# Optimization experiments

Hardware: AMD Instinct MI355X
Metric: run time of the kernel (lower is better)

Reference implementation:

```python
import jax, jax.numpy as jnp
import numpy as np

BAND_WIDTH = 0.5
EPS = 1e-5


def setup_inputs() -> dict:
    key = jax.random.key(0)
    k1, k2 = jax.random.split(key)
    shape = (8, 128, 16, 16, 16)  # (N, C, H, W, D)
    x = jax.random.normal(k1, shape, dtype=jnp.float32)
    y = jax.random.normal(k2, shape, dtype=jnp.float32)
    return {"x": x, "y": y}


def reference(x, y):
    N, C = x.shape[0], x.shape[1]
    L = x.shape[2] * x.shape[3] * x.shape[4]  # H*W*D
    xr = x.reshape(N, C, L)
    yr = y.reshape(N, C, L)
    # center by target mean over (batch, spatial)
    y_mu = yr.mean(axis=(0, 2), keepdims=True)  # (1, C, 1)
    xc = xr - y_mu
    yc = yr - y_mu
    # L2 normalize along channel dim (torch F.normalize: eps=1e-12 clamp on norm)
    xn = xc / jnp.maximum(jnp.linalg.norm(xc, axis=1, keepdims=True), 1e-12)
    yn = yc / jnp.maximum(jnp.linalg.norm(yc, axis=1, keepdims=True), 1e-12)
    # cosine similarity matrix (N, L, L): rows index x positions, cols y positions
    cos = jnp.einsum('ncl,ncm->nlm', xn, yn)
    dist = 1.0 - cos
    dist_min = jnp.min(dist, axis=2, keepdims=True)  # (N, L, 1)
    dist_tilde = dist / (dist_min + EPS)
    cx = jax.nn.softmax((1.0 - dist_tilde) / BAND_WIDTH, axis=2)
    cx = jnp.mean(jnp.max(cx, axis=1), axis=1)  # (N,)
    loss = jnp.mean(-jnp.log(cx + EPS))
    return loss
```

## Files before the change

kernel.cpp:

```cpp
#include <hip/hip_runtime.h>
#include <math.h>


#define NB 8
#define CC 128
#define LL 4096
#define CL (CC * LL)
#define EPSV 1e-5f
#define L2E 1.44269504f
#define TWO_L2E 2.88539008f

typedef __bf16 bf16x8 __attribute__((ext_vector_type(8)));
typedef float f32x4 __attribute__((ext_vector_type(4)));

__device__ __forceinline__ unsigned short f2bf(float f) {
    unsigned u = __float_as_uint(f);
    u += 0x7FFFu + ((u >> 16) & 1u);
    return (unsigned short)(u >> 16);
}

__global__ void k_mu1(const float* __restrict__ y, float* __restrict__ muP, float* __restrict__ out) {
    const int b = blockIdx.x;
    const int t = threadIdx.x;
    if (b == 0 && t == 0) out[0] = 0.f;
    const float* p = y + (size_t)b * LL;
    float4 v0 = *(const float4*)(p + t * 4);
    float4 v1 = *(const float4*)(p + 1024 + t * 4);
    float4 v2 = *(const float4*)(p + 2048 + t * 4);
    float4 v3 = *(const float4*)(p + 3072 + t * 4);
    float s = (v0.x + v0.y + v0.z + v0.w) + (v1.x + v1.y + v1.z + v1.w)
            + (v2.x + v2.y + v2.z + v2.w) + (v3.x + v3.y + v3.z + v3.w);
    for (int o = 1; o < 64; o <<= 1) s += __shfl_xor(s, o, 64);
    __shared__ float red[4];
    if ((t & 63) == 0) red[t >> 6] = s;
    __syncthreads();
    if (t == 0) muP[b] = (red[0] + red[1]) + (red[2] + red[3]);
}

__global__ __launch_bounds__(256, 2) void k_prep(const float* __restrict__ x, const float* __restrict__ y,
                                                 const float* __restrict__ muP,
                                                 unsigned short* __restrict__ xt, unsigned short* __restrict__ yt) {
    __shared__ float tf[CC][132];
    __shared__ float ssq[2][CC];
    __shared__ float invn[CC];
    __shared__ float mu_s[CC];
    const int b = blockIdx.x;
    const float* src = (b & 256) ? y : x;
    unsigned short* dst = (b & 256) ? yt : xt;
    const int sub = b & 255;
    const int n = sub >> 5, l0 = (sub & 31) << 7;
    const int t = threadIdx.x;
    if (t < CC) {
        float s = 0.f;
#pragma unroll
        for (int nn = 0; nn < NB; ++nn) s += muP[nn * CC + t];
        mu_s[t] = s * (1.0f / (float)(NB * LL));
    }
    const float* g = src + (size_t)n * CL + l0;
#pragma unroll
    for (int it = 0; it < 16; ++it) {
        int id = (it << 8) + t;
        int c = id >> 5, l4 = (id & 31) << 2;
        *(float4*)&tf[c][l4] = *(const float4*)(g + (size_t)c * LL + l4);
    }
    __syncthreads();
    {
        const int l = t & 127, half = t >> 7;
        float ss = 0.f;
#pragma unroll
        for (int cc = 0; cc < 64; ++cc) {
            int c = (half << 6) + cc;
            float v = tf[c][l] - mu_s[c];
            tf[c][l] = v;
            ss += v * v;
        }
        ssq[half][l] = ss;
    }
    __syncthreads();
    if (t < CC) invn[t] = 1.0f / fmaxf(sqrtf(ssq[0][t] + ssq[1][t]), 1e-12f);
    __syncthreads();
    unsigned short* o = dst + ((size_t)n * LL + l0) * CC;
#pragma unroll
    for (int it = 0; it < 8; ++it) {
        int id = (it << 8) + t;
        int lr = id >> 4, c8 = (id & 15) << 3;
        float w = invn[lr];
        unsigned short h[8] __attribute__((aligned(16)));
#pragma unroll
        for (int j = 0; j < 8; ++j) h[j] = f2bf(tf[c8 + j][lr] * w);
        *(uint4*)&o[(size_t)lr * CC + c8] = *(uint4*)h;
    }
}

__device__ __forceinline__ void stage_dma(const unsigned short* __restrict__ g,
                                          unsigned short* lds, int t) {
    const int w = t >> 6, ln = t & 63;
#pragma unroll
    for (int c = 0; c < 8; ++c) {
        int rbase = w * 32 + c * 4;
        int row = rbase + (ln >> 4);
        int gg = (ln & 15) ^ (row & 15);
        const unsigned short* gp = g + ((size_t)row << 7) + (gg << 3);
        __builtin_amdgcn_global_load_lds(
            (const __attribute__((address_space(1))) void*)gp,
            (__attribute__((address_space(3))) void*)(lds + (rbase << 7)),
            16, 0, 0);
    }
}

__device__ __forceinline__ bf16x8 ldsfrag(const unsigned short* lds, int r, int kq) {
    return *(const bf16x8*)&lds[(r << 7) + ((kq ^ (r & 15)) << 3)];
}

__device__ __forceinline__ void gather_frags(const unsigned short* __restrict__ g,
                                             bf16x8 (&areg)[4][4], int row0, int lane) {
    const int mr = lane & 15, q = lane >> 4;
    const unsigned short* ab = g + ((size_t)(row0 + mr) << 7) + q * 8;
#pragma unroll
    for (int k0i = 0; k0i < 4; ++k0i)
#pragma unroll
        for (int i = 0; i < 4; ++i)
            areg[k0i][i] = *(const bf16x8*)(ab + ((size_t)(i * 16) << 7) + k0i * 32);
}

__device__ __forceinline__ void mfma_stream(const bf16x8 (&areg)[4][4], const unsigned short* Bs,
                                            f32x4 (&acc)[4][4], int col0, int lane) {
    const int mr = lane & 15, q = lane >> 4;
#pragma unroll
    for (int k0i = 0; k0i < 4; ++k0i) {
        bf16x8 b[4];
#pragma unroll
        for (int j = 0; j < 4; ++j)
            b[j] = ldsfrag(Bs, col0 + j * 16 + mr, 4 * k0i + q);
#pragma unroll
        for (int i = 0; i < 4; ++i)
#pragma unroll
            for (int j = 0; j < 4; ++j)
                acc[i][j] = __builtin_amdgcn_mfma_f32_16x16x32_bf16(areg[k0i][i], b[j], acc[i][j], 0, 0, 0);
    }
}


#define DECODE_B(b, n_, lt_, ms_)                          \
    const int xcd_ = (b) & 7, slot_ = (b) >> 3;            \
    const int grp_ = xcd_ * 4 + (slot_ >> 5);              \
    const int n_ = grp_ >> 2, ms_ = grp_ & 3, lt_ = slot_ & 31;

__global__ __launch_bounds__(256, 2) void k_rowmax(const unsigned short* __restrict__ xt,
                                                   const unsigned short* __restrict__ yt,
                                                   float* __restrict__ rmP) {
    __shared__ unsigned short Bs[CC * CC];
    DECODE_B(blockIdx.x, n, lt, ms)
    const int t = threadIdx.x, lane = t & 63, w = t >> 6;
    const int row0 = (w & 1) << 6, col0 = (w >> 1) << 6;
    const int q = lane >> 4;
    bf16x8 areg[4][4];
    gather_frags(xt + ((size_t)(n * LL + lt * 128) << 7), areg, row0, lane);
    float rmax[16];
#pragma unroll
    for (int v = 0; v < 16; ++v) rmax[v] = -1e30f;
    for (int mt = ms * 8; mt < ms * 8 + 8; ++mt) {
        __syncthreads();
        stage_dma(yt + ((size_t)(n * LL + mt * 128) << 7), Bs, t);
        __syncthreads();
        f32x4 acc[4][4];
#pragma unroll
        for (int i = 0; i < 4; ++i)
#pragma unroll
            for (int j = 0; j < 4; ++j) acc[i][j] = 0.f;
        mfma_stream(areg, Bs, acc, col0, lane);
#pragma unroll
        for (int i = 0; i < 4; ++i)
#pragma unroll
            for (int r = 0; r < 4; ++r) {
                float m = acc[i][0][r];
#pragma unroll
                for (int j = 1; j < 4; ++j) m = fmaxf(m, acc[i][j][r]);
                rmax[i * 4 + r] = fmaxf(rmax[i * 4 + r], m);
            }
    }
#pragma unroll
    for (int v = 0; v < 16; ++v) {
        rmax[v] = fmaxf(rmax[v], __shfl_xor(rmax[v], 1, 64));
        rmax[v] = fmaxf(rmax[v], __shfl_xor(rmax[v], 2, 64));
        rmax[v] = fmaxf(rmax[v], __shfl_xor(rmax[v], 4, 64));
        rmax[v] = fmaxf(rmax[v], __shfl_xor(rmax[v], 8, 64));
    }
    if ((lane & 15) == 0) {
        const int part = ms * 2 + (w >> 1);
#pragma unroll
        for (int v = 0; v < 16; ++v) {
            int row = lt * 128 + row0 + (v >> 2) * 16 + q * 4 + (v & 3);
            rmP[((size_t)part << 15) + n * LL + row] = rmax[v];
        }
    }
}

__global__ __launch_bounds__(256, 2) void k_z(const unsigned short* __restrict__ xt,
                                              const unsigned short* __restrict__ yt,
                                              const float* __restrict__ rmP,
                                              float* __restrict__ Zp) {
    __shared__ unsigned short Bs[CC * CC];
    __shared__ float b2s[CC];
    DECODE_B(blockIdx.x, n, lt, ms)
    const int t = threadIdx.x, lane = t & 63, w = t >> 6;
    const int row0 = (w & 1) << 6, col0 = (w >> 1) << 6;
    const int q = lane >> 4;
    if (t < CC) {
        size_t gi = (size_t)n * LL + lt * 128 + t;
        float rm = -1e30f;
#pragma unroll
        for (int p = 0; p < 8; ++p) rm = fmaxf(rm, rmP[gi + ((size_t)p << 15)]);
        b2s[t] = (2.0f / (1.0f - rm + EPSV)) * L2E;
    }
    bf16x8 areg[4][4];
    gather_frags(xt + ((size_t)(n * LL + lt * 128) << 7), areg, row0, lane);
    __syncthreads();
    float b2[16], zs[16];
#pragma unroll
    for (int v = 0; v < 16; ++v) {
        b2[v] = b2s[row0 + (v >> 2) * 16 + q * 4 + (v & 3)];
        zs[v] = 0.f;
    }
    for (int mt = ms * 8; mt < ms * 8 + 8; ++mt) {
        __syncthreads();
        stage_dma(yt + ((size_t)(n * LL + mt * 128) << 7), Bs, t);
        __syncthreads();
        f32x4 acc[4][4];
#pragma unroll
        for (int i = 0; i < 4; ++i)
#pragma unroll
            for (int j = 0; j < 4; ++j) acc[i][j] = 0.f;
        mfma_stream(areg, Bs, acc, col0, lane);
#pragma unroll
        for (int i = 0; i < 4; ++i)
#pragma unroll
            for (int r = 0; r < 4; ++r) {
                int v = i * 4 + r;
                float e2v = TWO_L2E - b2[v];
                float s = 0.f;
#pragma unroll
                for (int j = 0; j < 4; ++j)
                    s += __builtin_amdgcn_exp2f(fmaf(b2[v], acc[i][j][r], e2v));
                zs[v] += s;
            }
    }
#pragma unroll
    for (int v = 0; v < 16; ++v) {
        zs[v] += __shfl_xor(zs[v], 1, 64);
        zs[v] += __shfl_xor(zs[v], 2, 64);
        zs[v] += __shfl_xor(zs[v], 4, 64);
        zs[v] += __shfl_xor(zs[v], 8, 64);
    }
    if ((lane & 15) == 0) {
        const int part = ms * 2 + (w >> 1);
#pragma unroll
        for (int v = 0; v < 16; ++v) {
            int row = lt * 128 + row0 + (v >> 2) * 16 + q * 4 + (v & 3);
            Zp[((size_t)part << 15) + n * LL + row] = zs[v];
        }
    }
}

__global__ __launch_bounds__(256, 2) void k_colmax(const unsigned short* __restrict__ xt,
                                                   const unsigned short* __restrict__ yt,
                                                   const float* __restrict__ rmP, const float* __restrict__ Zp,
                                                   float* __restrict__ cmP) {
    __shared__ unsigned short Bs[CC * CC];
    __shared__ float b2s[1024], g2s[1024];
    DECODE_B(blockIdx.x, n, ct, ls)
    const int t = threadIdx.x, lane = t & 63, w = t >> 6;
    const int row0 = (w & 1) << 6, col0 = (w >> 1) << 6;
    const int mr = lane & 15, q = lane >> 4;
    for (int i = t; i < 1024; i += 256) {
        size_t gi = (size_t)n * LL + ls * 1024 + i;
        float rm = -1e30f;
#pragma unroll
        for (int p = 0; p < 8; ++p) rm = fmaxf(rm, rmP[gi + ((size_t)p << 15)]);
        float b2 = (2.0f / (1.0f - rm + EPSV)) * L2E;
        float Z = 0.f;
#pragma unroll
        for (int p = 0; p < 8; ++p) Z += Zp[gi + ((size_t)p << 15)];
        b2s[i] = b2;
        g2s[i] = (TWO_L2E - b2) - __builtin_amdgcn_logf(Z);
    }
    bf16x8 areg[4][4];
    gather_frags(yt + ((size_t)(n * LL + ct * 128) << 7), areg, row0, lane);
    float cmax[16];
#pragma unroll
    for (int v = 0; v < 16; ++v) cmax[v] = -1e30f;
    for (int lt = ls * 8; lt < ls * 8 + 8; ++lt) {
        __syncthreads();
        stage_dma(xt + ((size_t)(n * LL + lt * 128) << 7), Bs, t);
        __syncthreads();
        f32x4 acc[4][4];
#pragma unroll
        for (int i = 0; i < 4; ++i)
#pragma unroll
            for (int j = 0; j < 4; ++j) acc[i][j] = 0.f;
        mfma_stream(areg, Bs, acc, col0, lane);
        float b2v[4], g2v[4];
        const int lbase = (lt - ls * 8) * 128 + col0 + mr;
#pragma unroll
        for (int j = 0; j < 4; ++j) {
            b2v[j] = b2s[lbase + j * 16];
            g2v[j] = g2s[lbase + j * 16];
        }
#pragma unroll
        for (int i = 0; i < 4; ++i)
#pragma unroll
            for (int r = 0; r < 4; ++r) {
                int v = i * 4 + r;
                float m = cmax[v];
#pragma unroll
                for (int j = 0; j < 4; ++j)
                    m = fmaxf(m, fmaf(b2v[j], acc[i][j][r], g2v[j]));
                cmax[v] = m;
            }
    }
#pragma unroll
    for (int v = 0; v < 16; ++v) {
        cmax[v] = fmaxf(cmax[v], __shfl_xor(cmax[v], 1, 64));
        cmax[v] = fmaxf(cmax[v], __shfl_xor(cmax[v], 2, 64));
        cmax[v] = fmaxf(cmax[v], __shfl_xor(cmax[v], 4, 64));
        cmax[v] = fmaxf(cmax[v], __shfl_xor(cmax[v], 8, 64));
    }
    if (mr == 0) {
        const int part = ls * 2 + (w >> 1);
#pragma unroll
        for (int v = 0; v < 16; ++v) {
            int yc = ct * 128 + row0 + (v >> 2) * 16 + q * 4 + (v & 3);
            cmP[((size_t)part << 15) + n * LL + yc] = cmax[v];
        }
    }
}

__global__ void k_loss(const float* __restrict__ cmP, float* __restrict__ out) {
    __shared__ float red[256];
    const int n = blockIdx.x, t = threadIdx.x;
    float s = 0.f;
    for (int m = t; m < LL; m += 256) {
        size_t idx = (size_t)n * LL + m;
        float e = -1e30f;
#pragma unroll
        for (int p = 0; p < 8; ++p) e = fmaxf(e, cmP[idx + ((size_t)p << 15)]);
        s += __builtin_amdgcn_exp2f(e);
    }
    red[t] = s;
    __syncthreads();
    for (int o = 128; o > 0; o >>= 1) {
        if (t < o) red[t] += red[t + o];
        __syncthreads();
    }
    if (t == 0)
        atomicAdd(out, -logf(red[0] * (1.0f / (float)LL) + EPSV) * (1.0f / (float)NB));
}

extern "C" void kernel_launch(void* const* d_in, const int* in_sizes, int n_in,
                              void* d_out, int out_size, void* d_ws, size_t ws_size,
                              hipStream_t stream) {
    const float* x = (const float*)d_in[0];
    const float* y = (const float*)d_in[1];
    float* out = (float*)d_out;
    char* ws = (char*)d_ws;

    unsigned short* xt = (unsigned short*)ws;
    unsigned short* yt = (unsigned short*)(ws + 8388608);
    char* p = ws + 16777216;
    float* muP = (float*)p;            p += 4096;
    float* rmP = (float*)p;            p += 8 * 131072;
    float* Zp  = (float*)p;            p += 8 * 131072;
    float* cmP = rmP;

    k_mu1<<<1024, 256, 0, stream>>>(y, muP, out);
    k_prep<<<512, 256, 0, stream>>>(x, y, muP, xt, yt);
    k_rowmax<<<1024, 256, 0, stream>>>(xt, yt, rmP);
    k_z<<<1024, 256, 0, stream>>>(xt, yt, rmP, Zp);
    k_colmax<<<1024, 256, 0, stream>>>(xt, yt, rmP, Zp, cmP);
    k_loss<<<8, 256, 0, stream>>>(cmP, out);
}
```

Measured before the change: 208.8 us.

## Load B fragments directly from global memory, halve grid with longer tile loops

Removes the LDS staging (global_load_lds DMA plus two barriers per tile) and has each wave read its B operand fragments straight from global memory. The three GEMM kernels now run 512 blocks, each covering 16 column tiles instead of 8, so the partial-result buffers shrink from 8 to 4 parts and cmP gets its own buffer. The goal is to drop barrier and LDS overhead, but B data is no longer shared through LDS, so L2 traffic rises and global load latency is exposed without double buffering.

```diff
diff --git a/kernel.cpp b/kernel.cpp
--- a/kernel.cpp
+++ b/kernel.cpp
@@ -92,26 +92,6 @@
     }
 }
 
-__device__ __forceinline__ void stage_dma(const unsigned short* __restrict__ g,
-                                          unsigned short* lds, int t) {
-    const int w = t >> 6, ln = t & 63;
-#pragma unroll
-    for (int c = 0; c < 8; ++c) {
-        int rbase = w * 32 + c * 4;
-        int row = rbase + (ln >> 4);
-        int gg = (ln & 15) ^ (row & 15);
-        const unsigned short* gp = g + ((size_t)row << 7) + (gg << 3);
-        __builtin_amdgcn_global_load_lds(
-            (const __attribute__((address_space(1))) void*)gp,
-            (__attribute__((address_space(3))) void*)(lds + (rbase << 7)),
-            16, 0, 0);
-    }
-}
-
-__device__ __forceinline__ bf16x8 ldsfrag(const unsigned short* lds, int r, int kq) {
-    return *(const bf16x8*)&lds[(r << 7) + ((kq ^ (r & 15)) << 3)];
-}
-
 __device__ __forceinline__ void gather_frags(const unsigned short* __restrict__ g,
                                              bf16x8 (&areg)[4][4], int row0, int lane) {
     const int mr = lane & 15, q = lane >> 4;
@@ -123,52 +103,50 @@
             areg[k0i][i] = *(const bf16x8*)(ab + ((size_t)(i * 16) << 7) + k0i * 32);
 }
 
-__device__ __forceinline__ void mfma_stream(const bf16x8 (&areg)[4][4], const unsigned short* Bs,
-                                            f32x4 (&acc)[4][4], int col0, int lane) {
-    const int mr = lane & 15, q = lane >> 4;
+__device__ __forceinline__ void mfma_direct(const bf16x8 (&areg)[4][4],
+                                            const unsigned short* __restrict__ bp,
+                                            f32x4 (&acc)[4][4]) {
 #pragma unroll
     for (int k0i = 0; k0i < 4; ++k0i) {
-        bf16x8 b[4];
+        bf16x8 bb[4];
 #pragma unroll
         for (int j = 0; j < 4; ++j)
-            b[j] = ldsfrag(Bs, col0 + j * 16 + mr, 4 * k0i + q);
+            bb[j] = *(const bf16x8*)(bp + ((size_t)(j * 16) << 7) + k0i * 32);
 #pragma unroll
         for (int i = 0; i < 4; ++i)
 #pragma unroll
             for (int j = 0; j < 4; ++j)
-                acc[i][j] = __builtin_amdgcn_mfma_f32_16x16x32_bf16(areg[k0i][i], b[j], acc[i][j], 0, 0, 0);
-    }
-}
-
-
-#define DECODE_B(b, n_, lt_, ms_)                          \
+                acc[i][j] = __builtin_amdgcn_mfma_f32_16x16x32_bf16(areg[k0i][i], bb[j], acc[i][j], 0, 0, 0);
+    }
+}
+
+
+#define DECODE_512(b, n_, lt_, ms_)                        \
     const int xcd_ = (b) & 7, slot_ = (b) >> 3;            \
-    const int grp_ = xcd_ * 4 + (slot_ >> 5);              \
-    const int n_ = grp_ >> 2, ms_ = grp_ & 3, lt_ = slot_ & 31;
+    const int grp_ = xcd_ * 2 + (slot_ >> 5);              \
+    const int n_ = grp_ >> 1, ms_ = grp_ & 1, lt_ = slot_ & 31;
 
 __global__ __launch_bounds__(256, 2) void k_rowmax(const unsigned short* __restrict__ xt,
                                                    const unsigned short* __restrict__ yt,
                                                    float* __restrict__ rmP) {
-    __shared__ unsigned short Bs[CC * CC];
-    DECODE_B(blockIdx.x, n, lt, ms)
+    DECODE_512(blockIdx.x, n, lt, ms)
     const int t = threadIdx.x, lane = t & 63, w = t >> 6;
     const int row0 = (w & 1) << 6, col0 = (w >> 1) << 6;
-    const int q = lane >> 4;
+    const int mr = lane & 15, q = lane >> 4;
     bf16x8 areg[4][4];
     gather_frags(xt + ((size_t)(n * LL + lt * 128) << 7), areg, row0, lane);
     float rmax[16];
 #pragma unroll
     for (int v = 0; v < 16; ++v) rmax[v] = -1e30f;
-    for (int mt = ms * 8; mt < ms * 8 + 8; ++mt) {
-        __syncthreads();
-        stage_dma(yt + ((size_t)(n * LL + mt * 128) << 7), Bs, t);
-        __syncthreads();
+    const unsigned short* ybase = yt + ((size_t)(n * LL + col0 + mr) << 7) + q * 8;
+    for (int mt = ms * 16; mt < ms * 16 + 16; ++mt) {
+        const unsigned short* bp = ybase + ((size_t)(mt * 128) << 7);
         f32x4 acc[4][4];
 #pragma unroll
         for (int i = 0; i < 4; ++i)
 #pragma unroll
             for (int j = 0; j < 4; ++j) acc[i][j] = 0.f;
-        mfma_stream(areg, Bs, acc, col0, lane);
+        mfma_direct(areg, bp, acc);
 #pragma unroll
         for (int i = 0; i < 4; ++i)
 #pragma unroll
@@ -200,17 +178,16 @@
                                               const unsigned short* __restrict__ yt,
                                               const float* __restrict__ rmP,
                                               float* __restrict__ Zp) {
-    __shared__ unsigned short Bs[CC * CC];
     __shared__ float b2s[CC];
-    DECODE_B(blockIdx.x, n, lt, ms)
+    DECODE_512(blockIdx.x, n, lt, ms)
     const int t = threadIdx.x, lane = t & 63, w = t >> 6;
     const int row0 = (w & 1) << 6, col0 = (w >> 1) << 6;
-    const int q = lane >> 4;
+    const int mr = lane & 15, q = lane >> 4;
     if (t < CC) {
         size_t gi = (size_t)n * LL + lt * 128 + t;
         float rm = -1e30f;
 #pragma unroll
-        for (int p = 0; p < 8; ++p) rm = fmaxf(rm, rmP[gi + ((size_t)p << 15)]);
+        for (int p = 0; p < 4; ++p) rm = fmaxf(rm, rmP[gi + ((size_t)p << 15)]);
         b2s[t] = (2.0f / (1.0f - rm + EPSV)) * L2E;
     }
     bf16x8 areg[4][4];
@@ -222,16 +199,15 @@
         b2[v] = b2s[row0 + (v >> 2) * 16 + q * 4 + (v & 3)];
         zs[v] = 0.f;
     }
-    for (int mt = ms * 8; mt < ms * 8 + 8; ++mt) {
-        __syncthreads();
-        stage_dma(yt + ((size_t)(n * LL + mt * 128) << 7), Bs, t);
-        __syncthreads();
+    const unsigned short* ybase = yt + ((size_t)(n * LL + col0 + mr) << 7) + q * 8;
+    for (int mt = ms * 16; mt < ms * 16 + 16; ++mt) {
+        const unsigned short* bp = ybase + ((size_t)(mt * 128) << 7);
         f32x4 acc[4][4];
 #pragma unroll
         for (int i = 0; i < 4; ++i)
 #pragma unroll
             for (int j = 0; j < 4; ++j) acc[i][j] = 0.f;
-        mfma_stream(areg, Bs, acc, col0, lane);
+        mfma_direct(areg, bp, acc);
 #pragma unroll
         for (int i = 0; i < 4; ++i)
 #pragma unroll
@@ -266,41 +242,40 @@
                                                    const unsigned short* __restrict__ yt,
                                                    const float* __restrict__ rmP, const float* __restrict__ Zp,
                                                    float* __restrict__ cmP) {
-    __shared__ unsigned short Bs[CC * CC];
-    __shared__ float b2s[1024], g2s[1024];
-    DECODE_B(blockIdx.x, n, ct, ls)
+    __shared__ float b2s[2048], g2s[2048];
+    DECODE_512(blockIdx.x, n, ct, ls)
     const int t = threadIdx.x, lane = t & 63, w = t >> 6;
     const int row0 = (w & 1) << 6, col0 = (w >> 1) << 6;
     const int mr = lane & 15, q = lane >> 4;
-    for (int i = t; i < 1024; i += 256) {
-        size_t gi = (size_t)n * LL + ls * 1024 + i;
+    for (int i = t; i < 2048; i += 256) {
+        size_t gi = (size_t)n * LL + ls * 2048 + i;
         float rm = -1e30f;
 #pragma unroll
-        for (int p = 0; p < 8; ++p) rm = fmaxf(rm, rmP[gi + ((size_t)p << 15)]);
+        for (int p = 0; p < 4; ++p) rm = fmaxf(rm, rmP[gi + ((size_t)p << 15)]);
         float b2 = (2.0f / (1.0f - rm + EPSV)) * L2E;
         float Z = 0.f;
 #pragma unroll
-        for (int p = 0; p < 8; ++p) Z += Zp[gi + ((size_t)p << 15)];
+        for (int p = 0; p < 4; ++p) Z += Zp[gi + ((size_t)p << 15)];
         b2s[i] = b2;
         g2s[i] = (TWO_L2E - b2) - __builtin_amdgcn_logf(Z);
     }
     bf16x8 areg[4][4];
     gather_frags(yt + ((size_t)(n * LL + ct * 128) << 7), areg, row0, lane);
+    __syncthreads();
     float cmax[16];
 #pragma unroll
     for (int v = 0; v < 16; ++v) cmax[v] = -1e30f;
-    for (int lt = ls * 8; lt < ls * 8 + 8; ++lt) {
-        __syncthreads();
-        stage_dma(xt + ((size_t)(n * LL + lt * 128) << 7), Bs, t);
-        __syncthreads();
+    const unsigned short* xbase = xt + ((size_t)(n * LL + col0 + mr) << 7) + q * 8;
+    for (int lt = ls * 16; lt < ls * 16 + 16; ++lt) {
+        const unsigned short* bp = xbase + ((size_t)(lt * 128) << 7);
         f32x4 acc[4][4];
 #pragma unroll
         for (int i = 0; i < 4; ++i)
 #pragma unroll
             for (int j = 0; j < 4; ++j) acc[i][j] = 0.f;
-        mfma_stream(areg, Bs, acc, col0, lane);
+        mfma_direct(areg, bp, acc);
         float b2v[4], g2v[4];
-        const int lbase = (lt - ls * 8) * 128 + col0 + mr;
+        const int lbase = (lt - ls * 16) * 128 + col0 + mr;
 #pragma unroll
         for (int j = 0; j < 4; ++j) {
             b2v[j] = b2s[lbase + j * 16];
@@ -343,7 +318,7 @@
         size_t idx = (size_t)n * LL + m;
         float e = -1e30f;
 #pragma unroll
-        for (int p = 0; p < 8; ++p) e = fmaxf(e, cmP[idx + ((size_t)p << 15)]);
+        for (int p = 0; p < 4; ++p) e = fmaxf(e, cmP[idx + ((size_t)p << 15)]);
         s += __builtin_amdgcn_exp2f(e);
     }
     red[t] = s;
@@ -368,14 +343,14 @@
     unsigned short* yt = (unsigned short*)(ws + 8388608);
     char* p = ws + 16777216;
     float* muP = (float*)p;            p += 4096;
-    float* rmP = (float*)p;            p += 8 * 131072;
-    float* Zp  = (float*)p;            p += 8 * 131072;
-    float* cmP = rmP;
+    float* rmP = (float*)p;            p += 4 * 131072;
+    float* Zp  = (float*)p;            p += 4 * 131072;
+    float* cmP = (float*)p;            p += 4 * 131072;
 
     k_mu1<<<1024, 256, 0, stream>>>(y, muP, out);
     k_prep<<<512, 256, 0, stream>>>(x, y, muP, xt, yt);
-    k_rowmax<<<1024, 256, 0, stream>>>(xt, yt, rmP);
-    k_z<<<1024, 256, 0, stream>>>(xt, yt, rmP, Zp);
-    k_colmax<<<1024, 256, 0, stream>>>(xt, yt, rmP, Zp, cmP);
+    k_rowmax<<<512, 256, 0, stream>>>(xt, yt, rmP);
+    k_z<<<512, 256, 0, stream>>>(xt, yt, rmP, Zp);
+    k_colmax<<<512, 256, 0, stream>>>(xt, yt, rmP, Zp, cmP);
     k_loss<<<8, 256, 0, stream>>>(cmP, out);
 }
```

Result: slower. 290.4 us (+39.1%).

## Double-buffer LDS tiles with async DMA prefetch in the three GEMM passes

Applied to the files above, without the earlier changes.

Converts the single shared-memory B tile into two buffers in the rowmax, Z and colmax kernels, prefetching the tile two iterations ahead and waiting on a partial vmcnt before a raw barrier. This is meant to overlap the global-to-LDS copy of the next y or x tile with the MFMA work on the current one, removing the full sync-load-sync stall each iteration. LDS use doubles to 64KB per block, which may limit occupancy to one block per CU despite the launch bound of 2. The colmax output moves to a separate buffer so it no longer aliases rmP while rmP is still being read.

```diff
diff --git a/kernel.cpp b/kernel.cpp
--- a/kernel.cpp
+++ b/kernel.cpp
@@ -140,6 +140,15 @@
     }
 }
 
+#define PIPE_WAIT_BARRIER() do {                                   \
+    asm volatile("s_waitcnt vmcnt(8)" ::: "memory");               \
+    __builtin_amdgcn_s_barrier();                                  \
+} while (0)
+#define PIPE_RELEASE_BARRIER() do {                                \
+    asm volatile("" ::: "memory");                                 \
+    __builtin_amdgcn_s_barrier();                                  \
+} while (0)
+
 
 #define DECODE_B(b, n_, lt_, ms_)                          \
     const int xcd_ = (b) & 7, slot_ = (b) >> 3;            \
@@ -149,35 +158,41 @@
 __global__ __launch_bounds__(256, 2) void k_rowmax(const unsigned short* __restrict__ xt,
                                                    const unsigned short* __restrict__ yt,
                                                    float* __restrict__ rmP) {
-    __shared__ unsigned short Bs[CC * CC];
+    __shared__ unsigned short Bs[2][CC * CC];
     DECODE_B(blockIdx.x, n, lt, ms)
     const int t = threadIdx.x, lane = t & 63, w = t >> 6;
     const int row0 = (w & 1) << 6, col0 = (w >> 1) << 6;
     const int q = lane >> 4;
+    const unsigned short* ytn = yt + ((size_t)n * LL << 7);
     bf16x8 areg[4][4];
     gather_frags(xt + ((size_t)(n * LL + lt * 128) << 7), areg, row0, lane);
     float rmax[16];
 #pragma unroll
     for (int v = 0; v < 16; ++v) rmax[v] = -1e30f;
-    for (int mt = ms * 8; mt < ms * 8 + 8; ++mt) {
-        __syncthreads();
-        stage_dma(yt + ((size_t)(n * LL + mt * 128) << 7), Bs, t);
-        __syncthreads();
+    const int mt0 = ms * 8;
+    stage_dma(ytn + ((size_t)(mt0 * 128) << 7), Bs[0], t);
+    stage_dma(ytn + ((size_t)((mt0 + 1) * 128) << 7), Bs[1], t);
+    int pb = 0;
+    for (int i = 0; i < 8; ++i) {
+        PIPE_WAIT_BARRIER();
         f32x4 acc[4][4];
 #pragma unroll
-        for (int i = 0; i < 4; ++i)
-#pragma unroll
-            for (int j = 0; j < 4; ++j) acc[i][j] = 0.f;
-        mfma_stream(areg, Bs, acc, col0, lane);
-#pragma unroll
-        for (int i = 0; i < 4; ++i)
+        for (int ii = 0; ii < 4; ++ii)
+#pragma unroll
+            for (int j = 0; j < 4; ++j) acc[ii][j] = 0.f;
+        mfma_stream(areg, Bs[pb], acc, col0, lane);
+#pragma unroll
+        for (int ii = 0; ii < 4; ++ii)
 #pragma unroll
             for (int r = 0; r < 4; ++r) {
-                float m = acc[i][0][r];
-#pragma unroll
-                for (int j = 1; j < 4; ++j) m = fmaxf(m, acc[i][j][r]);
-                rmax[i * 4 + r] = fmaxf(rmax[i * 4 + r], m);
+                float m = acc[ii][0][r];
+#pragma unroll
+                for (int j = 1; j < 4; ++j) m = fmaxf(m, acc[ii][j][r]);
+                rmax[ii * 4 + r] = fmaxf(rmax[ii * 4 + r], m);
             }
+        PIPE_RELEASE_BARRIER();
+        if (i + 2 < 8) stage_dma(ytn + ((size_t)((mt0 + i + 2) * 128) << 7), Bs[pb], t);
+        pb ^= 1;
     }
 #pragma unroll
     for (int v = 0; v < 16; ++v) {
@@ -200,7 +215,7 @@
                                               const unsigned short* __restrict__ yt,
                                               const float* __restrict__ rmP,
                                               float* __restrict__ Zp) {
-    __shared__ unsigned short Bs[CC * CC];
+    __shared__ unsigned short Bs[2][CC * CC];
     __shared__ float b2s[CC];
     DECODE_B(blockIdx.x, n, lt, ms)
     const int t = threadIdx.x, lane = t & 63, w = t >> 6;
@@ -222,26 +237,32 @@
         b2[v] = b2s[row0 + (v >> 2) * 16 + q * 4 + (v & 3)];
         zs[v] = 0.f;
     }
-    for (int mt = ms * 8; mt < ms * 8 + 8; ++mt) {
-        __syncthreads();
-        stage_dma(yt + ((size_t)(n * LL + mt * 128) << 7), Bs, t);
-        __syncthreads();
+    const unsigned short* ytn = yt + ((size_t)n * LL << 7);
+    const int mt0 = ms * 8;
+    stage_dma(ytn + ((size_t)(mt0 * 128) << 7), Bs[0], t);
+    stage_dma(ytn + ((size_t)((mt0 + 1) * 128) << 7), Bs[1], t);
+    int pb = 0;
+    for (int i = 0; i < 8; ++i) {
+        PIPE_WAIT_BARRIER();
         f32x4 acc[4][4];
 #pragma unroll
-        for (int i = 0; i < 4; ++i)
-#pragma unroll
-            for (int j = 0; j < 4; ++j) acc[i][j] = 0.f;
-        mfma_stream(areg, Bs, acc, col0, lane);
-#pragma unroll
-        for (int i = 0; i < 4; ++i)
+        for (int ii = 0; ii < 4; ++ii)
+#pragma unroll
+            for (int j = 0; j < 4; ++j) acc[ii][j] = 0.f;
+        mfma_stream(areg, Bs[pb], acc, col0, lane);
+        PIPE_RELEASE_BARRIER();
+        if (i + 2 < 8) stage_dma(ytn + ((size_t)((mt0 + i + 2) * 128) << 7), Bs[pb], t);
+        pb ^= 1;
+#pragma unroll
+        for (int ii = 0; ii < 4; ++ii)
 #pragma unroll
             for (int r = 0; r < 4; ++r) {
-                int v = i * 4 + r;
+                int v = ii * 4 + r;
                 float e2v = TWO_L2E - b2[v];
                 float s = 0.f;
 #pragma unroll
                 for (int j = 0; j < 4; ++j)
-                    s += __builtin_amdgcn_exp2f(fmaf(b2[v], acc[i][j][r], e2v));
+                    s += __builtin_amdgcn_exp2f(fmaf(b2[v], acc[ii][j][r], e2v));
                 zs[v] += s;
             }
     }
@@ -266,7 +287,7 @@
                                                    const unsigned short* __restrict__ yt,
                                                    const float* __restrict__ rmP, const float* __restrict__ Zp,
                                                    float* __restrict__ cmP) {
-    __shared__ unsigned short Bs[CC * CC];
+    __shared__ unsigned short Bs[2][CC * CC];
     __shared__ float b2s[1024], g2s[1024];
     DECODE_B(blockIdx.x, n, ct, ls)
     const int t = threadIdx.x, lane = t & 63, w = t >> 6;
@@ -286,35 +307,42 @@
     }
     bf16x8 areg[4][4];
     gather_frags(yt + ((size_t)(n * LL + ct * 128) << 7), areg, row0, lane);
+    __syncthreads();
     float cmax[16];
 #pragma unroll
     for (int v = 0; v < 16; ++v) cmax[v] = -1e30f;
-    for (int lt = ls * 8; lt < ls * 8 + 8; ++lt) {
-        __syncthreads();
-        stage_dma(xt + ((size_t)(n * LL + lt * 128) << 7), Bs, t);
-        __syncthreads();
+    const unsigned short* xtn = xt + ((size_t)n * LL << 7);
+    const int lt0 = ls * 8;
+    stage_dma(xtn + ((size_t)(lt0 * 128) << 7), Bs[0], t);
+    stage_dma(xtn + ((size_t)((lt0 + 1) * 128) << 7), Bs[1], t);
+    int pb = 0;
+    for (int i = 0; i < 8; ++i) {
+        PIPE_WAIT_BARRIER();
         f32x4 acc[4][4];
 #pragma unroll
-        for (int i = 0; i < 4; ++i)
-#pragma unroll
-            for (int j = 0; j < 4; ++j) acc[i][j] = 0.f;
-        mfma_stream(areg, Bs, acc, col0, lane);
+        for (int ii = 0; ii < 4; ++ii)
+#pragma unroll
+            for (int j = 0; j < 4; ++j) acc[ii][j] = 0.f;
+        mfma_stream(areg, Bs[pb], acc, col0, lane);
+        PIPE_RELEASE_BARRIER();
+        if (i + 2 < 8) stage_dma(xtn + ((size_t)((lt0 + i + 2) * 128) << 7), Bs[pb], t);
+        pb ^= 1;
         float b2v[4], g2v[4];
-        const int lbase = (lt - ls * 8) * 128 + col0 + mr;
+        const int lbase = i * 128 + col0 + mr;
 #pragma unroll
         for (int j = 0; j < 4; ++j) {
             b2v[j] = b2s[lbase + j * 16];
             g2v[j] = g2s[lbase + j * 16];
         }
 #pragma unroll
-        for (int i = 0; i < 4; ++i)
+        for (int ii = 0; ii < 4; ++ii)
 #pragma unroll
             for (int r = 0; r < 4; ++r) {
-                int v = i * 4 + r;
+                int v = ii * 4 + r;
                 float m = cmax[v];
 #pragma unroll
                 for (int j = 0; j < 4; ++j)
-                    m = fmaxf(m, fmaf(b2v[j], acc[i][j][r], g2v[j]));
+                    m = fmaxf(m, fmaf(b2v[j], acc[ii][j][r], g2v[j]));
                 cmax[v] = m;
             }
     }
@@ -370,7 +398,7 @@
     float* muP = (float*)p;            p += 4096;
     float* rmP = (float*)p;            p += 8 * 131072;
     float* Zp  = (float*)p;            p += 8 * 131072;
-    float* cmP = rmP;
+    float* cmP = (float*)p;            p += 8 * 131072;
 
     k_mu1<<<1024, 256, 0, stream>>>(y, muP, out);
     k_prep<<<512, 256, 0, stream>>>(x, y, muP, xt, yt);
```

After: 209.4 us. No clear change (+0.3%).

## Retile similarity GEMM kernels to 32-row warp strips with 64-column LDS tiles

Applied to the files above, without the earlier changes.

Each warp now owns a 32×64 output strip instead of a 64×64 quadrant, and the staged B tile shrinks from 128 to 64 rows. This halves LDS use and the accumulator/fragment register footprint, so launch bounds can ask for 3 blocks per CU to raise occupancy. Partial results now come from 4 partitions instead of 8, and cmP gets its own buffer instead of aliasing rmP. In exchange each warp reuses its A fragments over fewer columns, and each block does twice as many barrier-synchronised staging rounds.

```diff
diff --git a/kernel.cpp b/kernel.cpp
--- a/kernel.cpp
+++ b/kernel.cpp
@@ -92,12 +92,12 @@
     }
 }
 
-__device__ __forceinline__ void stage_dma(const unsigned short* __restrict__ g,
-                                          unsigned short* lds, int t) {
+__device__ __forceinline__ void stage_dma64(const unsigned short* __restrict__ g,
+                                            unsigned short* lds, int t) {
     const int w = t >> 6, ln = t & 63;
 #pragma unroll
-    for (int c = 0; c < 8; ++c) {
-        int rbase = w * 32 + c * 4;
+    for (int c = 0; c < 4; ++c) {
+        int rbase = w * 16 + c * 4;
         int row = rbase + (ln >> 4);
         int gg = (ln & 15) ^ (row & 15);
         const unsigned short* gp = g + ((size_t)row << 7) + (gg << 3);
@@ -112,28 +112,28 @@
     return *(const bf16x8*)&lds[(r << 7) + ((kq ^ (r & 15)) << 3)];
 }
 
-__device__ __forceinline__ void gather_frags(const unsigned short* __restrict__ g,
-                                             bf16x8 (&areg)[4][4], int row0, int lane) {
+__device__ __forceinline__ void gather_frags32(const unsigned short* __restrict__ g,
+                                               bf16x8 (&areg)[4][2], int row0, int lane) {
     const int mr = lane & 15, q = lane >> 4;
     const unsigned short* ab = g + ((size_t)(row0 + mr) << 7) + q * 8;
 #pragma unroll
     for (int k0i = 0; k0i < 4; ++k0i)
 #pragma unroll
-        for (int i = 0; i < 4; ++i)
+        for (int i = 0; i < 2; ++i)
             areg[k0i][i] = *(const bf16x8*)(ab + ((size_t)(i * 16) << 7) + k0i * 32);
 }
 
-__device__ __forceinline__ void mfma_stream(const bf16x8 (&areg)[4][4], const unsigned short* Bs,
-                                            f32x4 (&acc)[4][4], int col0, int lane) {
+__device__ __forceinline__ void mfma_stream32(const bf16x8 (&areg)[4][2], const unsigned short* Bs,
+                                              f32x4 (&acc)[2][4], int lane) {
     const int mr = lane & 15, q = lane >> 4;
 #pragma unroll
     for (int k0i = 0; k0i < 4; ++k0i) {
         bf16x8 b[4];
 #pragma unroll
         for (int j = 0; j < 4; ++j)
-            b[j] = ldsfrag(Bs, col0 + j * 16 + mr, 4 * k0i + q);
-#pragma unroll
-        for (int i = 0; i < 4; ++i)
+            b[j] = ldsfrag(Bs, j * 16 + mr, 4 * k0i + q);
+#pragma unroll
+        for (int i = 0; i < 2; ++i)
 #pragma unroll
             for (int j = 0; j < 4; ++j)
                 acc[i][j] = __builtin_amdgcn_mfma_f32_16x16x32_bf16(areg[k0i][i], b[j], acc[i][j], 0, 0, 0);
@@ -146,31 +146,32 @@
     const int grp_ = xcd_ * 4 + (slot_ >> 5);              \
     const int n_ = grp_ >> 2, ms_ = grp_ & 3, lt_ = slot_ & 31;
 
-__global__ __launch_bounds__(256, 2) void k_rowmax(const unsigned short* __restrict__ xt,
+__global__ __launch_bounds__(256, 3) void k_rowmax(const unsigned short* __restrict__ xt,
                                                    const unsigned short* __restrict__ yt,
                                                    float* __restrict__ rmP) {
-    __shared__ unsigned short Bs[CC * CC];
+    __shared__ unsigned short Bs[64 * CC];
     DECODE_B(blockIdx.x, n, lt, ms)
     const int t = threadIdx.x, lane = t & 63, w = t >> 6;
-    const int row0 = (w & 1) << 6, col0 = (w >> 1) << 6;
-    const int q = lane >> 4;
-    bf16x8 areg[4][4];
-    gather_frags(xt + ((size_t)(n * LL + lt * 128) << 7), areg, row0, lane);
-    float rmax[16];
-#pragma unroll
-    for (int v = 0; v < 16; ++v) rmax[v] = -1e30f;
-    for (int mt = ms * 8; mt < ms * 8 + 8; ++mt) {
-        __syncthreads();
-        stage_dma(yt + ((size_t)(n * LL + mt * 128) << 7), Bs, t);
-        __syncthreads();
-        f32x4 acc[4][4];
-#pragma unroll
-        for (int i = 0; i < 4; ++i)
+    const int row0 = w << 5;
+    const int mr = lane & 15, q = lane >> 4;
+    bf16x8 areg[4][2];
+    gather_frags32(xt + ((size_t)(n * LL + lt * 128) << 7) + ((size_t)row0 << 7) - ((size_t)row0 << 7),
+                   areg, row0, lane);
+    float rmax[8];
+#pragma unroll
+    for (int v = 0; v < 8; ++v) rmax[v] = -1e30f;
+    for (int mt = ms * 16; mt < ms * 16 + 16; ++mt) {
+        __syncthreads();
+        stage_dma64(yt + ((size_t)(n * LL + mt * 64) << 7), Bs, t);
+        __syncthreads();
+        f32x4 acc[2][4];
+#pragma unroll
+        for (int i = 0; i < 2; ++i)
 #pragma unroll
             for (int j = 0; j < 4; ++j) acc[i][j] = 0.f;
-        mfma_stream(areg, Bs, acc, col0, lane);
-#pragma unroll
-        for (int i = 0; i < 4; ++i)
+        mfma_stream32(areg, Bs, acc, lane);
+#pragma unroll
+        for (int i = 0; i < 2; ++i)
 #pragma unroll
             for (int r = 0; r < 4; ++r) {
                 float m = acc[i][0][r];
@@ -180,60 +181,59 @@
             }
     }
 #pragma unroll
-    for (int v = 0; v < 16; ++v) {
+    for (int v = 0; v < 8; ++v) {
         rmax[v] = fmaxf(rmax[v], __shfl_xor(rmax[v], 1, 64));
         rmax[v] = fmaxf(rmax[v], __shfl_xor(rmax[v], 2, 64));
         rmax[v] = fmaxf(rmax[v], __shfl_xor(rmax[v], 4, 64));
         rmax[v] = fmaxf(rmax[v], __shfl_xor(rmax[v], 8, 64));
     }
-    if ((lane & 15) == 0) {
-        const int part = ms * 2 + (w >> 1);
-#pragma unroll
-        for (int v = 0; v < 16; ++v) {
+    if (mr == 0) {
+#pragma unroll
+        for (int v = 0; v < 8; ++v) {
             int row = lt * 128 + row0 + (v >> 2) * 16 + q * 4 + (v & 3);
-            rmP[((size_t)part << 15) + n * LL + row] = rmax[v];
-        }
-    }
-}
-
-__global__ __launch_bounds__(256, 2) void k_z(const unsigned short* __restrict__ xt,
+            rmP[((size_t)ms << 15) + n * LL + row] = rmax[v];
+        }
+    }
+}
+
+__global__ __launch_bounds__(256, 3) void k_z(const unsigned short* __restrict__ xt,
                                               const unsigned short* __restrict__ yt,
                                               const float* __restrict__ rmP,
                                               float* __restrict__ Zp) {
-    __shared__ unsigned short Bs[CC * CC];
+    __shared__ unsigned short Bs[64 * CC];
     __shared__ float b2s[CC];
     DECODE_B(blockIdx.x, n, lt, ms)
     const int t = threadIdx.x, lane = t & 63, w = t >> 6;
-    const int row0 = (w & 1) << 6, col0 = (w >> 1) << 6;
-    const int q = lane >> 4;
+    const int row0 = w << 5;
+    const int mr = lane & 15, q = lane >> 4;
     if (t < CC) {
         size_t gi = (size_t)n * LL + lt * 128 + t;
         float rm = -1e30f;
 #pragma unroll
-        for (int p = 0; p < 8; ++p) rm = fmaxf(rm, rmP[gi + ((size_t)p << 15)]);
+        for (int p = 0; p < 4; ++p) rm = fmaxf(rm, rmP[gi + ((size_t)p << 15)]);
         b2s[t] = (2.0f / (1.0f - rm + EPSV)) * L2E;
     }
-    bf16x8 areg[4][4];
-    gather_frags(xt + ((size_t)(n * LL + lt * 128) << 7), areg, row0, lane);
-    __syncthreads();
-    float b2[16], zs[16];
-#pragma unroll
-    for (int v = 0; v < 16; ++v) {
+    bf16x8 areg[4][2];
+    gather_frags32(xt + ((size_t)(n * LL + lt * 128) << 7), areg, row0, lane);
+    __syncthreads();
+    float b2[8], zs[8];
+#pragma unroll
+    for (int v = 0; v < 8; ++v) {
         b2[v] = b2s[row0 + (v >> 2) * 16 + q * 4 + (v & 3)];
         zs[v] = 0.f;
     }
-    for (int mt = ms * 8; mt < ms * 8 + 8; ++mt) {
-        __syncthreads();
-        stage_dma(yt + ((size_t)(n * LL + mt * 128) << 7), Bs, t);
-        __syncthreads();
-        f32x4 acc[4][4];
-#pragma unroll
-        for (int i = 0; i < 4; ++i)
+    for (int mt = ms * 16; mt < ms * 16 + 16; ++mt) {
+        __syncthreads();
+        stage_dma64(yt + ((size_t)(n * LL + mt * 64) << 7), Bs, t);
+        __syncthreads();
+        f32x4 acc[2][4];
+#pragma unroll
+        for (int i = 0; i < 2; ++i)
 #pragma unroll
             for (int j = 0; j < 4; ++j) acc[i][j] = 0.f;
-        mfma_stream(areg, Bs, acc, col0, lane);
-#pragma unroll
-        for (int i = 0; i < 4; ++i)
+        mfma_stream32(areg, Bs, acc, lane);
+#pragma unroll
+        for (int i = 0; i < 2; ++i)
 #pragma unroll
             for (int r = 0; r < 4; ++r) {
                 int v = i * 4 + r;
@@ -246,68 +246,68 @@
             }
     }
 #pragma unroll
-    for (int v = 0; v < 16; ++v) {
+    for (int v = 0; v < 8; ++v) {
         zs[v] += __shfl_xor(zs[v], 1, 64);
         zs[v] += __shfl_xor(zs[v], 2, 64);
         zs[v] += __shfl_xor(zs[v], 4, 64);
         zs[v] += __shfl_xor(zs[v], 8, 64);
     }
-    if ((lane & 15) == 0) {
-        const int part = ms * 2 + (w >> 1);
-#pragma unroll
-        for (int v = 0; v < 16; ++v) {
+    if (mr == 0) {
+#pragma unroll
+        for (int v = 0; v < 8; ++v) {
             int row = lt * 128 + row0 + (v >> 2) * 16 + q * 4 + (v & 3);
-            Zp[((size_t)part << 15) + n * LL + row] = zs[v];
-        }
-    }
-}
-
-__global__ __launch_bounds__(256, 2) void k_colmax(const unsigned short* __restrict__ xt,
+            Zp[((size_t)ms << 15) + n * LL + row] = zs[v];
+        }
+    }
+}
+
+__global__ __launch_bounds__(256, 3) void k_colmax(const unsigned short* __restrict__ xt,
                                                    const unsigned short* __restrict__ yt,
                                                    const float* __restrict__ rmP, const float* __restrict__ Zp,
                                                    float* __restrict__ cmP) {
-    __shared__ unsigned short Bs[CC * CC];
+    __shared__ unsigned short Bs[64 * CC];
     __shared__ float b2s[1024], g2s[1024];
     DECODE_B(blockIdx.x, n, ct, ls)
     const int t = threadIdx.x, lane = t & 63, w = t >> 6;
-    const int row0 = (w & 1) << 6, col0 = (w >> 1) << 6;
+    const int row0 = w << 5;
     const int mr = lane & 15, q = lane >> 4;
     for (int i = t; i < 1024; i += 256) {
         size_t gi = (size_t)n * LL + ls * 1024 + i;
         float rm = -1e30f;
 #pragma unroll
-        for (int p = 0; p < 8; ++p) rm = fmaxf(rm, rmP[gi + ((size_t)p << 15)]);
+        for (int p = 0; p < 4; ++p) rm = fmaxf(rm, rmP[gi + ((size_t)p << 15)]);
         float b2 = (2.0f / (1.0f - rm + EPSV)) * L2E;
         float Z = 0.f;
 #pragma unroll
-        for (int p = 0; p < 8; ++p) Z += Zp[gi + ((size_t)p << 15)];
+        for (int p = 0; p < 4; ++p) Z += Zp[gi + ((size_t)p << 15)];
         b2s[i] = b2;
         g2s[i] = (TWO_L2E - b2) - __builtin_amdgcn_logf(Z);
     }
-    bf16x8 areg[4][4];
-    gather_frags(yt + ((size_t)(n * LL + ct * 128) << 7), areg, row0, lane);
-    float cmax[16];
-#pragma unroll
-    for (int v = 0; v < 16; ++v) cmax[v] = -1e30f;
-    for (int lt = ls * 8; lt < ls * 8 + 8; ++lt) {
-        __syncthreads();
-        stage_dma(xt + ((size_t)(n * LL + lt * 128) << 7), Bs, t);
-        __syncthreads();
-        f32x4 acc[4][4];
-#pragma unroll
-        for (int i = 0; i < 4; ++i)
+    bf16x8 areg[4][2];
+    gather_frags32(yt + ((size_t)(n * LL + ct * 128) << 7), areg, row0, lane);
+    __syncthreads();
+    float cmax[8];
+#pragma unroll
+    for (int v = 0; v < 8; ++v) cmax[v] = -1e30f;
+    for (int lt = ls * 16; lt < ls * 16 + 16; ++lt) {
+        __syncthreads();
+        stage_dma64(xt + ((size_t)(n * LL + lt * 64) << 7), Bs, t);
+        __syncthreads();
+        f32x4 acc[2][4];
+#pragma unroll
+        for (int i = 0; i < 2; ++i)
 #pragma unroll
             for (int j = 0; j < 4; ++j) acc[i][j] = 0.f;
-        mfma_stream(areg, Bs, acc, col0, lane);
+        mfma_stream32(areg, Bs, acc, lane);
         float b2v[4], g2v[4];
-        const int lbase = (lt - ls * 8) * 128 + col0 + mr;
+        const int lbase = (lt - ls * 16) * 64 + mr;
 #pragma unroll
         for (int j = 0; j < 4; ++j) {
             b2v[j] = b2s[lbase + j * 16];
             g2v[j] = g2s[lbase + j * 16];
         }
 #pragma unroll
-        for (int i = 0; i < 4; ++i)
+        for (int i = 0; i < 2; ++i)
 #pragma unroll
             for (int r = 0; r < 4; ++r) {
                 int v = i * 4 + r;
@@ -319,18 +319,17 @@
             }
     }
 #pragma unroll
-    for (int v = 0; v < 16; ++v) {
+    for (int v = 0; v < 8; ++v) {
         cmax[v] = fmaxf(cmax[v], __shfl_xor(cmax[v], 1, 64));
         cmax[v] = fmaxf(cmax[v], __shfl_xor(cmax[v], 2, 64));
         cmax[v] = fmaxf(cmax[v], __shfl_xor(cmax[v], 4, 64));
         cmax[v] = fmaxf(cmax[v], __shfl_xor(cmax[v], 8, 64));
     }
     if (mr == 0) {
-        const int part = ls * 2 + (w >> 1);
-#pragma unroll
-        for (int v = 0; v < 16; ++v) {
+#pragma unroll
+        for (int v = 0; v < 8; ++v) {
             int yc = ct * 128 + row0 + (v >> 2) * 16 + q * 4 + (v & 3);
-            cmP[((size_t)part << 15) + n * LL + yc] = cmax[v];
+            cmP[((size_t)ls << 15) + n * LL + yc] = cmax[v];
         }
     }
 }
@@ -343,7 +342,7 @@
         size_t idx = (size_t)n * LL + m;
         float e = -1e30f;
 #pragma unroll
-        for (int p = 0; p < 8; ++p) e = fmaxf(e, cmP[idx + ((size_t)p << 15)]);
+        for (int p = 0; p < 4; ++p) e = fmaxf(e, cmP[idx + ((size_t)p << 15)]);
         s += __builtin_amdgcn_exp2f(e);
     }
     red[t] = s;
@@ -368,9 +367,9 @@
     unsigned short* yt = (unsigned short*)(ws + 8388608);
     char* p = ws + 16777216;
     float* muP = (float*)p;            p += 4096;
-    float* rmP = (float*)p;            p += 8 * 131072;
-    float* Zp  = (float*)p;            p += 8 * 131072;
-    float* cmP = rmP;
+    float* rmP = (float*)p;            p += 4 * 131072;
+    float* Zp  = (float*)p;            p += 4 * 131072;
+    float* cmP = (float*)p;            p += 4 * 131072;
 
     k_mu1<<<1024, 256, 0, stream>>>(y, muP, out);
     k_prep<<<512, 256, 0, stream>>>(x, y, muP, xt, yt);
```

Result: faster. 191.9 us (-8.1%).
